# Performance work log

Hardware: AMD Instinct MI355X
Metric: run time of the kernel (lower is better)

The kernel has to match this reference:

```python
import jax, jax.numpy as jnp
import numpy as np

TOPK = 8
EXTRA = 0  # ADDITIONAL_LAYERS_IN_GPU
CPU_TOPK = int(0.25 * 64)  # CPU_MOE_RATIO * num_experts = 16


def setup_inputs() -> dict:
    key = jax.random.key(0)
    k1, k2 = jax.random.split(key)
    hidden_states = jax.random.normal(k1, (4, 4096, 4096), dtype=jnp.float32)
    wg_weight = jax.random.normal(k2, (64, 4096), dtype=jnp.float32) * 0.02
    return {"hidden_states": hidden_states, "wg_weight": wg_weight}


def reference(hidden_states, wg_weight):
    bsz, seq_len, hidden_size = hidden_states.shape
    x = hidden_states.reshape(-1, hidden_size).astype(jnp.float32)  # [T, H]
    logits = jnp.einsum('th,eh->te', x, wg_weight)  # [T, 64]
    gates = jax.nn.softmax(logits, axis=1)
    values_all, indices_all = jax.lax.top_k(gates, TOPK + EXTRA)
    expert_weight = values_all[:, :TOPK]
    expert_index = indices_all[:, :TOPK]
    _, cpu_expert_index = jax.lax.top_k(gates, CPU_TOPK)
    cpu_expert_index = cpu_expert_index[:, 8 + EXTRA:]
    # norm_topk_prob=True, topk > 1
    eps = jnp.finfo(jnp.float32).eps
    denom = jnp.maximum(expert_weight.sum(axis=1, keepdims=True), eps)
    expert_weight = expert_weight / denom
    return (expert_weight, expert_index, cpu_expert_index, indices_all)
```

## Files before the change

kernel.cpp:

```cpp
#include <hip/hip_runtime.h>

#define T_TOK 16384
#define HDIM  4096
#define NEXP  64
#define TAU   2e-4f
#define BM    128

typedef unsigned short u16;
typedef u16   u16x8  __attribute__((ext_vector_type(8)));
typedef __bf16 bf16x8 __attribute__((ext_vector_type(8)));
typedef float f32x4  __attribute__((ext_vector_type(4)));

__device__ __forceinline__ u16 f2bf(float f) {
    unsigned u = __builtin_bit_cast(unsigned, f);
    unsigned r = u + 0x7FFFu + ((u >> 16) & 1u);
    return (u16)(r >> 16);
}
__device__ __forceinline__ float bf2f(u16 h) {
    unsigned u = ((unsigned)h) << 16;
    return __builtin_bit_cast(float, u);
}

__global__ void zero_counter(int* counter) {
    if (threadIdx.x == 0) counter[0] = 0;
}

__global__ __launch_bounds__(256)
void wsplit_kernel(const float* __restrict__ w, u16x8* __restrict__ wfrag,
                   float4* __restrict__ wt4) {
    const int id  = blockIdx.x * 256 + threadIdx.x;
    const int e   = id >> 9;
    const int k8g = id & 511;
    const int k   = k8g * 8;

    const float* wp = w + (size_t)e * HDIM + k;
    const float4 v0 = *(const float4*)wp;
    const float4 v1 = *(const float4*)(wp + 4);

    wt4[(size_t)(2 * k8g) * NEXP + e]     = v0;
    wt4[(size_t)(2 * k8g + 1) * NEXP + e] = v1;

    const float fv[8] = {v0.x, v0.y, v0.z, v0.w, v1.x, v1.y, v1.z, v1.w};
    u16x8 hv, lv;
#pragma unroll
    for (int j = 0; j < 8; ++j) {
        const u16 h = f2bf(fv[j]);
        hv[j] = h;
        lv[j] = f2bf(fv[j] - bf2f(h));
    }
    const int chunk = k >> 6;
    const int k8 = (k >> 3) & 7, ks = k8 >> 2, g = k8 & 3, nt = e >> 4;
    const int U = ks * 256 + nt * 64 + 16 * g + (e & 15);
    const int q = U ^ k8;
    wfrag[(size_t)chunk * 1024 + q]       = hv;
    wfrag[(size_t)chunk * 1024 + 512 + q] = lv;
}

__global__ __launch_bounds__(256, 3)
void gate_gemm_mfma(const float* __restrict__ x, const u16x8* __restrict__ wfrag,
                    float* __restrict__ partial, int ksplit) {
    const int b      = blockIdx.x;
    const int kslice = b % ksplit;
    const int tblk   = b / ksplit;
    const int kspan  = HDIM / ksplit;
    const int k0     = kslice * kspan;
    const int t0     = tblk * BM;

    __shared__ __align__(16) u16 smem[3072 * 8];

    const int tid  = threadIdx.x;
    const int lane = tid & 63;
    const int wv   = tid >> 6;

    f32x4 acc[2][4];
#pragma unroll
    for (int m = 0; m < 2; ++m)
#pragma unroll
        for (int nt = 0; nt < 4; ++nt) acc[m][nt] = (f32x4){0.f, 0.f, 0.f, 0.f};

    u16x8  wreg[4];
    float4 xr0[4], xr1[4];

    auto issue = [&](int kc) {
        const u16x8* ws = wfrag + (size_t)(kc >> 6) * 1024;
#pragma unroll
        for (int i = 0; i < 4; ++i) wreg[i] = ws[tid + 256 * i];
#pragma unroll
        for (int i = 0; i < 4; ++i) {
            const int L = tid + 256 * i;
            const int row = L >> 3, k8 = L & 7;
            const float* xp = x + (size_t)(t0 + row) * HDIM + kc + 8 * k8;
            xr0[i] = *(const float4*)xp;
            xr1[i] = *(const float4*)(xp + 4);
        }
    };

    issue(k0);

    for (int kc = k0; kc < k0 + kspan; kc += 64) {
        __syncthreads();

#pragma unroll
        for (int i = 0; i < 4; ++i)
            *(u16x8*)(smem + (size_t)(tid + 256 * i) * 8) = wreg[i];
#pragma unroll
        for (int i = 0; i < 4; ++i) {
            const int L = tid + 256 * i, row = L >> 3, k8 = L & 7;
            const float fv[8] = {xr0[i].x, xr0[i].y, xr0[i].z, xr0[i].w,
                                 xr1[i].x, xr1[i].y, xr1[i].z, xr1[i].w};
            u16x8 hv, lv;
#pragma unroll
            for (int j = 0; j < 8; ++j) {
                const u16 h = f2bf(fv[j]);
                hv[j] = h;
                lv[j] = f2bf(fv[j] - bf2f(h));
            }
            const int g = k8 & 3, ks = k8 >> 2, mt = row >> 4;
            const int U = ks * 512 + mt * 64 + 16 * g + (row & 15);
            const int phys = U ^ k8;
            *(u16x8*)(smem + (size_t)(1024 + phys) * 8) = hv;
            *(u16x8*)(smem + (size_t)(2048 + phys) * 8) = lv;
        }

        if (kc + 64 < k0 + kspan) issue(kc + 64);

        __syncthreads();

#pragma unroll
        for (int ks = 0; ks < 2; ++ks) {
            const int xo = (ks << 2) + (lane >> 4);
            bf16x8 axh[2], axl[2];
#pragma unroll
            for (int m = 0; m < 2; ++m) {
                const int ux = (ks * 512 + (wv * 2 + m) * 64 + lane) ^ xo;
                axh[m] = __builtin_bit_cast(bf16x8, *(const u16x8*)(smem + (size_t)(1024 + ux) * 8));
                axl[m] = __builtin_bit_cast(bf16x8, *(const u16x8*)(smem + (size_t)(2048 + ux) * 8));
            }
#pragma unroll
            for (int nt = 0; nt < 4; ++nt) {
                const int uw = (ks * 256 + nt * 64 + lane) ^ xo;
                const bf16x8 bh = __builtin_bit_cast(bf16x8, *(const u16x8*)(smem + (size_t)uw * 8));
                const bf16x8 bl = __builtin_bit_cast(bf16x8, *(const u16x8*)(smem + (size_t)(512 + uw) * 8));
#pragma unroll
                for (int m = 0; m < 2; ++m) {
                    acc[m][nt] = __builtin_amdgcn_mfma_f32_16x16x32_bf16(axh[m], bh, acc[m][nt], 0, 0, 0);
                    acc[m][nt] = __builtin_amdgcn_mfma_f32_16x16x32_bf16(axh[m], bl, acc[m][nt], 0, 0, 0);
                    acc[m][nt] = __builtin_amdgcn_mfma_f32_16x16x32_bf16(axl[m], bh, acc[m][nt], 0, 0, 0);
                }
            }
        }
    }

    float* op = partial + (size_t)kslice * T_TOK * NEXP;
    const int ecol = lane & 15;
#pragma unroll
    for (int m = 0; m < 2; ++m) {
        const int trow = t0 + (wv * 2 + m) * 16 + ((lane >> 4) << 2);
#pragma unroll
        for (int nt = 0; nt < 4; ++nt)
#pragma unroll
            for (int r = 0; r < 4; ++r)
                op[(size_t)(trow + r) * NEXP + nt * 16 + ecol] = acc[m][nt][r];
    }
}

__global__ __launch_bounds__(256)
void gate_topk_f32(const float* __restrict__ partial, int ksplit,
                   float* __restrict__ out, int* __restrict__ list,
                   int* __restrict__ counter) {
    const int wave = threadIdx.x >> 6;
    const int lane = threadIdx.x & 63;
    const int t = blockIdx.x * 4 + wave;

    float l = 0.f;
    for (int s = 0; s < ksplit; ++s)
        l += partial[(size_t)s * T_TOK * NEXP + (size_t)t * NEXP + lane];

    float v = l;
    const int idx = lane;
    float myval = -3.4e38f;
    int   myidx = 0;
#pragma unroll
    for (int r = 0; r < 17; ++r) {
        float bv = v;
        int   bi = idx;
#pragma unroll
        for (int s = 1; s < 64; s <<= 1) {
            const float ov = __shfl_xor(bv, s);
            const int   oi = __shfl_xor(bi, s);
            if (ov > bv || (ov == bv && oi < bi)) { bv = ov; bi = oi; }
        }
        if (lane == r) { myval = bv; myidx = bi; }
        if (idx == bi) v = -3.4e38f;
    }

    const float nxt = __shfl(myval, (lane + 1) & 63);
    const bool close = (lane < 16) && (myval - nxt < TAU);
    if (__ballot(close) != 0ull) {
        if (lane == 0) { const int p = atomicAdd(counter, 1); list[p] = t; }
    }

    const float m = __shfl(myval, 0);
    const float p = (lane < 16) ? expf(myval - m) : 0.f;
    float s8 = (lane < 8) ? p : 0.f;
#pragma unroll
    for (int s = 1; s < 64; s <<= 1) s8 += __shfl_xor(s8, s);

    float* ew = out;
    float* ei = out + (size_t)T_TOK * 8;
    float* ci = out + (size_t)2 * T_TOK * 8;
    float* ia = out + (size_t)3 * T_TOK * 8;
    if (lane < 8) {
        ew[(size_t)t * 8 + lane] = p / s8;
        ei[(size_t)t * 8 + lane] = (float)myidx;
        ia[(size_t)t * 8 + lane] = (float)myidx;
    } else if (lane < 16) {
        ci[(size_t)t * 8 + (lane - 8)] = (float)myidx;
    }
}

__global__ __launch_bounds__(256)
void repair_partial(const float* __restrict__ x, const float4* __restrict__ wt4,
                    const int* __restrict__ list, const int* __restrict__ counter,
                    double* __restrict__ fpart) {
    const int lane = threadIdx.x & 63;
    const int wid  = (int)((blockIdx.x * blockDim.x + threadIdx.x) >> 6);
    const int nw   = (int)((gridDim.x * blockDim.x) >> 6);
    const int nit  = counter[0] * 16;

    for (int it = wid; it < nit; it += nw) {
        const int li = it >> 4;
        const int ks = it & 15;
        const int t  = __builtin_amdgcn_readfirstlane(list[li]);
        const float4* xr4 = (const float4*)(x + (size_t)t * HDIM) + ks * 64;
        const float4* wb  = wt4 + (size_t)ks * 64 * NEXP;

        double a0 = 0.0, a1 = 0.0, a2 = 0.0, a3 = 0.0;
#pragma unroll 4
        for (int j = 0; j < 64; j += 4) {
            const float4 w0 = wb[(size_t)(j + 0) * NEXP + lane];
            const float4 w1 = wb[(size_t)(j + 1) * NEXP + lane];
            const float4 w2 = wb[(size_t)(j + 2) * NEXP + lane];
            const float4 w3 = wb[(size_t)(j + 3) * NEXP + lane];
            const float4 x0 = xr4[j + 0];
            const float4 x1 = xr4[j + 1];
            const float4 x2 = xr4[j + 2];
            const float4 x3 = xr4[j + 3];
            a0 = fma((double)x0.x, (double)w0.x, a0);
            a0 = fma((double)x0.y, (double)w0.y, a0);
            a0 = fma((double)x0.z, (double)w0.z, a0);
            a0 = fma((double)x0.w, (double)w0.w, a0);
            a1 = fma((double)x1.x, (double)w1.x, a1);
            a1 = fma((double)x1.y, (double)w1.y, a1);
            a1 = fma((double)x1.z, (double)w1.z, a1);
            a1 = fma((double)x1.w, (double)w1.w, a1);
            a2 = fma((double)x2.x, (double)w2.x, a2);
            a2 = fma((double)x2.y, (double)w2.y, a2);
            a2 = fma((double)x2.z, (double)w2.z, a2);
            a2 = fma((double)x2.w, (double)w2.w, a2);
            a3 = fma((double)x3.x, (double)w3.x, a3);
            a3 = fma((double)x3.y, (double)w3.y, a3);
            a3 = fma((double)x3.z, (double)w3.z, a3);
            a3 = fma((double)x3.w, (double)w3.w, a3);
        }
        fpart[(size_t)li * 1024 + ks * 64 + lane] = (a0 + a1) + (a2 + a3);
    }
}

__global__ __launch_bounds__(256)
void repair_final(const double* __restrict__ fpart, const int* __restrict__ list,
                  const int* __restrict__ counter, float* __restrict__ out) {
    const int lane = threadIdx.x & 63;
    const int wid  = (int)((blockIdx.x * blockDim.x + threadIdx.x) >> 6);
    const int nw   = (int)((gridDim.x * blockDim.x) >> 6);
    const int n    = counter[0];

    for (int li = wid; li < n; li += nw) {
        const int t = __builtin_amdgcn_readfirstlane(list[li]);

        double v = 0.0;
#pragma unroll
        for (int ks = 0; ks < 16; ++ks)
            v += fpart[(size_t)li * 1024 + ks * 64 + lane];

        const int idx = lane;
        double mylog = -1.0e308;
        int    myidx = 0;
#pragma unroll
        for (int r = 0; r < 16; ++r) {
            double bv = v;
            int    bi = idx;
#pragma unroll
            for (int s = 1; s < 64; s <<= 1) {
                const double ov = __shfl_xor(bv, s);
                const int    oi = __shfl_xor(bi, s);
                if (ov > bv || (ov == bv && oi < bi)) { bv = ov; bi = oi; }
            }
            if (lane == r) { mylog = bv; myidx = bi; }
            if (idx == bi) v = -1.0e308;
        }

        const double m = __shfl(mylog, 0);
        const float p = (lane < 16) ? expf((float)(mylog - m)) : 0.f;
        float s8 = (lane < 8) ? p : 0.f;
#pragma unroll
        for (int s = 1; s < 64; s <<= 1) s8 += __shfl_xor(s8, s);

        float* ew = out;
        float* ei = out + (size_t)T_TOK * 8;
        float* ci = out + (size_t)2 * T_TOK * 8;
        float* ia = out + (size_t)3 * T_TOK * 8;
        if (lane < 8) {
            ew[(size_t)t * 8 + lane] = p / s8;
            ei[(size_t)t * 8 + lane] = (float)myidx;
            ia[(size_t)t * 8 + lane] = (float)myidx;
        } else if (lane < 16) {
            ci[(size_t)t * 8 + (lane - 8)] = (float)myidx;
        }
    }
}

extern "C" void kernel_launch(void* const* d_in, const int* in_sizes, int n_in,
                              void* d_out, int out_size, void* d_ws, size_t ws_size,
                              hipStream_t stream) {
    const float* x = (const float*)d_in[0];
    const float* w = (const float*)d_in[1];
    float* out     = (float*)d_out;

    const size_t slice      = (size_t)T_TOK * NEXP * sizeof(float);
    const size_t wfragBytes = (size_t)64 * 1024 * 16;
    const size_t wt4Bytes   = (size_t)NEXP * HDIM * sizeof(float);
    const size_t fpartBytes = (size_t)T_TOK * 16 * NEXP * sizeof(double);
    const size_t extra      = wfragBytes + wt4Bytes + fpartBytes +
                              (size_t)T_TOK * sizeof(int) + 64;

    int ksplit = 1;
    if      (ws_size >= 4 * slice + extra) ksplit = 4;
    else if (ws_size >= 2 * slice + extra) ksplit = 2;

    float*  partial = (float*)d_ws;
    u16x8*  wfrag   = (u16x8*)((char*)d_ws + (size_t)ksplit * slice);
    float4* wt4     = (float4*)((char*)wfrag + wfragBytes);
    double* fpart   = (double*)((char*)wt4 + wt4Bytes);
    int*    list    = (int*)((char*)fpart + fpartBytes);
    int*    counter = list + T_TOK;

    zero_counter<<<1, 64, 0, stream>>>(counter);
    wsplit_kernel<<<128, 256, 0, stream>>>(w, wfrag, wt4);
    gate_gemm_mfma<<<ksplit * (T_TOK / BM), 256, 0, stream>>>(x, wfrag, partial, ksplit);
    gate_topk_f32<<<T_TOK / 4, 256, 0, stream>>>(partial, ksplit, out, list, counter);
    repair_partial<<<4096, 256, 0, stream>>>(x, wt4, list, counter, fpart);
    repair_final<<<1024, 256, 0, stream>>>(fpart, list, counter, out);
}
```

Measured before the change: 155.2 us.

## Read weight fragments directly from global memory and drop register prefetch

The GEMM kernel no longer stages gate-weight fragments in shared memory. Each wave reads its B fragments straight from the precomputed unswizzled global layout, which is small and cache-resident, so shared memory per block drops and launch bounds rise to 4 blocks per CU. The register-held prefetch of the next x tile is removed, and manual bf16 rounding is replaced with native __bf16 conversions. The trade is lost overlap of global x loads with compute and repeated L2/L1 weight reads per wave, in exchange for higher occupancy and fewer LDS writes.

```diff
diff --git a/kernel.cpp b/kernel.cpp
--- a/kernel.cpp
+++ b/kernel.cpp
@@ -10,16 +10,6 @@
 typedef u16   u16x8  __attribute__((ext_vector_type(8)));
 typedef __bf16 bf16x8 __attribute__((ext_vector_type(8)));
 typedef float f32x4  __attribute__((ext_vector_type(4)));
-
-__device__ __forceinline__ u16 f2bf(float f) {
-    unsigned u = __builtin_bit_cast(unsigned, f);
-    unsigned r = u + 0x7FFFu + ((u >> 16) & 1u);
-    return (u16)(r >> 16);
-}
-__device__ __forceinline__ float bf2f(u16 h) {
-    unsigned u = ((unsigned)h) << 16;
-    return __builtin_bit_cast(float, u);
-}
 
 __global__ void zero_counter(int* counter) {
     if (threadIdx.x == 0) counter[0] = 0;
@@ -41,22 +31,21 @@
     wt4[(size_t)(2 * k8g + 1) * NEXP + e] = v1;
 
     const float fv[8] = {v0.x, v0.y, v0.z, v0.w, v1.x, v1.y, v1.z, v1.w};
-    u16x8 hv, lv;
+    bf16x8 hv, lv;
 #pragma unroll
     for (int j = 0; j < 8; ++j) {
-        const u16 h = f2bf(fv[j]);
+        const __bf16 h = (__bf16)fv[j];
         hv[j] = h;
-        lv[j] = f2bf(fv[j] - bf2f(h));
+        lv[j] = (__bf16)(fv[j] - (float)h);
     }
     const int chunk = k >> 6;
     const int k8 = (k >> 3) & 7, ks = k8 >> 2, g = k8 & 3, nt = e >> 4;
     const int U = ks * 256 + nt * 64 + 16 * g + (e & 15);
-    const int q = U ^ k8;
-    wfrag[(size_t)chunk * 1024 + q]       = hv;
-    wfrag[(size_t)chunk * 1024 + 512 + q] = lv;
-}
-
-__global__ __launch_bounds__(256, 3)
+    wfrag[(size_t)chunk * 1024 + U]       = __builtin_bit_cast(u16x8, hv);
+    wfrag[(size_t)chunk * 1024 + 512 + U] = __builtin_bit_cast(u16x8, lv);
+}
+
+__global__ __launch_bounds__(256, 4)
 void gate_gemm_mfma(const float* __restrict__ x, const u16x8* __restrict__ wfrag,
                     float* __restrict__ partial, int ksplit) {
     const int b      = blockIdx.x;
@@ -66,7 +55,8 @@
     const int k0     = kslice * kspan;
     const int t0     = tblk * BM;
 
-    __shared__ __align__(16) u16 smem[3072 * 8];
+    __shared__ __align__(16) u16 smem[2048 * 8];
+    u16x8* smemv = (u16x8*)smem;
 
     const int tid  = threadIdx.x;
     const int lane = tid & 63;
@@ -78,69 +68,49 @@
 #pragma unroll
         for (int nt = 0; nt < 4; ++nt) acc[m][nt] = (f32x4){0.f, 0.f, 0.f, 0.f};
 
-    u16x8  wreg[4];
-    float4 xr0[4], xr1[4];
-
-    auto issue = [&](int kc) {
-        const u16x8* ws = wfrag + (size_t)(kc >> 6) * 1024;
-#pragma unroll
-        for (int i = 0; i < 4; ++i) wreg[i] = ws[tid + 256 * i];
-#pragma unroll
-        for (int i = 0; i < 4; ++i) {
-            const int L = tid + 256 * i;
-            const int row = L >> 3, k8 = L & 7;
-            const float* xp = x + (size_t)(t0 + row) * HDIM + kc + 8 * k8;
-            xr0[i] = *(const float4*)xp;
-            xr1[i] = *(const float4*)(xp + 4);
-        }
-    };
-
-    issue(k0);
-
     for (int kc = k0; kc < k0 + kspan; kc += 64) {
         __syncthreads();
 
 #pragma unroll
-        for (int i = 0; i < 4; ++i)
-            *(u16x8*)(smem + (size_t)(tid + 256 * i) * 8) = wreg[i];
-#pragma unroll
         for (int i = 0; i < 4; ++i) {
-            const int L = tid + 256 * i, row = L >> 3, k8 = L & 7;
-            const float fv[8] = {xr0[i].x, xr0[i].y, xr0[i].z, xr0[i].w,
-                                 xr1[i].x, xr1[i].y, xr1[i].z, xr1[i].w};
-            u16x8 hv, lv;
+            const int L   = tid + 256 * i;
+            const int row = L >> 3;
+            const int k8  = L & 7;
+            const float* xp = x + (size_t)(t0 + row) * HDIM + kc + 8 * k8;
+            const float4 v0 = *(const float4*)xp;
+            const float4 v1 = *(const float4*)(xp + 4);
+            const float fv[8] = {v0.x, v0.y, v0.z, v0.w, v1.x, v1.y, v1.z, v1.w};
+            bf16x8 hv, lv;
 #pragma unroll
             for (int j = 0; j < 8; ++j) {
-                const u16 h = f2bf(fv[j]);
+                const __bf16 h = (__bf16)fv[j];
                 hv[j] = h;
-                lv[j] = f2bf(fv[j] - bf2f(h));
+                lv[j] = (__bf16)(fv[j] - (float)h);
             }
             const int g = k8 & 3, ks = k8 >> 2, mt = row >> 4;
             const int U = ks * 512 + mt * 64 + 16 * g + (row & 15);
             const int phys = U ^ k8;
-            *(u16x8*)(smem + (size_t)(1024 + phys) * 8) = hv;
-            *(u16x8*)(smem + (size_t)(2048 + phys) * 8) = lv;
-        }
-
-        if (kc + 64 < k0 + kspan) issue(kc + 64);
-
+            smemv[phys]        = __builtin_bit_cast(u16x8, hv);
+            smemv[1024 + phys] = __builtin_bit_cast(u16x8, lv);
+        }
         __syncthreads();
 
-#pragma unroll
-        for (int ks = 0; ks < 2; ++ks) {
-            const int xo = (ks << 2) + (lane >> 4);
+        const u16x8* wsrc = wfrag + (size_t)(kc >> 6) * 1024;
+#pragma unroll
+        for (int ks2 = 0; ks2 < 2; ++ks2) {
+            const int xo = (ks2 << 2) + (lane >> 4);
             bf16x8 axh[2], axl[2];
 #pragma unroll
             for (int m = 0; m < 2; ++m) {
-                const int ux = (ks * 512 + (wv * 2 + m) * 64 + lane) ^ xo;
-                axh[m] = __builtin_bit_cast(bf16x8, *(const u16x8*)(smem + (size_t)(1024 + ux) * 8));
-                axl[m] = __builtin_bit_cast(bf16x8, *(const u16x8*)(smem + (size_t)(2048 + ux) * 8));
+                const int ux = (ks2 * 512 + (wv * 2 + m) * 64 + lane) ^ xo;
+                axh[m] = __builtin_bit_cast(bf16x8, smemv[ux]);
+                axl[m] = __builtin_bit_cast(bf16x8, smemv[1024 + ux]);
             }
 #pragma unroll
             for (int nt = 0; nt < 4; ++nt) {
-                const int uw = (ks * 256 + nt * 64 + lane) ^ xo;
-                const bf16x8 bh = __builtin_bit_cast(bf16x8, *(const u16x8*)(smem + (size_t)uw * 8));
-                const bf16x8 bl = __builtin_bit_cast(bf16x8, *(const u16x8*)(smem + (size_t)(512 + uw) * 8));
+                const int uwi = ks2 * 256 + nt * 64 + lane;
+                const bf16x8 bh = __builtin_bit_cast(bf16x8, wsrc[uwi]);
+                const bf16x8 bl = __builtin_bit_cast(bf16x8, wsrc[512 + uwi]);
 #pragma unroll
                 for (int m = 0; m < 2; ++m) {
                     acc[m][nt] = __builtin_amdgcn_mfma_f32_16x16x32_bf16(axh[m], bh, acc[m][nt], 0, 0, 0);
```

Result: slower. 177.5 us (+14.4%).
